# Kernel tuning notes

Measured on AMD Instinct MI355X. Metric: run time of the kernel, lower is better.

## Reference

```python
import jax, jax.numpy as jnp
import numpy as np

NO = 16          # config['Max_Object']
NT = 8           # config['Max_Time']
FEAT = 512       # config['feat_dims']
VIS_IN = 2048
TGT = 24


def setup_inputs() -> dict:
    key = jax.random.key(0)
    ks = jax.random.split(key, 10)
    b = 16
    N = NT * 2 * NO  # 256
    s = lambda k, *sh: jax.random.normal(k, sh, dtype=jnp.float32) * 0.02
    return {
        "src": jax.random.normal(ks[0], (b, 1, 1, N, VIS_IN), dtype=jnp.float32),
        "tgt_rel": jax.random.randint(ks[1], (b * NT * NO * NO,), 0, TGT, dtype=jnp.int64),
        "w1": s(ks[2], VIS_IN, FEAT), "b1": jnp.zeros((FEAT,), jnp.float32),
        "w2": s(ks[3], FEAT, FEAT),   "b2": jnp.zeros((FEAT,), jnp.float32),
        "wf": s(ks[4], FEAT, FEAT),   "bf": jnp.zeros((FEAT,), jnp.float32),
        "wr": s(ks[5], 2 * FEAT, TGT), "br": jnp.zeros((TGT,), jnp.float32),
    }


def reference(src, tgt_rel, w1, b1, w2, b2, wf, bf, wr, br):
    b = src.shape[0]
    BT = b * NT
    # src[:, 0, 0, :, :] -> (b, N, D) -> (b*NT, 2*NO, D); take visual part [:2048]
    x = src[:, 0, 0, :, :].reshape(BT, 2 * NO, -1)[:, :, :VIS_IN]
    # fc_vis: MLP 2048 -> FEAT -> FEAT
    h = jnp.maximum(x @ w1 + b1, 0.0) @ w2 + b2          # (BT, 2NO, FEAT)
    node_feats = h @ wf + bf                             # fc_fusion
    # vectorized replacement of the NOxNO python double loop:
    # edge[:, i*NO + (j-NO), :] = cat(node[:, i], node[:, j])  for i<NO<=j
    subj = jnp.broadcast_to(node_feats[:, :NO, None, :], (BT, NO, NO, FEAT))
    obj = jnp.broadcast_to(node_feats[:, None, NO:, :], (BT, NO, NO, FEAT))
    edge_feats = jnp.concatenate([subj, obj], axis=-1).reshape(BT, NO * NO, 2 * FEAT)
    out = (edge_feats @ wr + br).reshape(-1, TGT)        # fc_rel
    tgt = tgt_rel.reshape(-1)
    w_cls = jnp.asarray([1.0] + [100.0] * (TGT - 1), dtype=out.dtype)
    logp = jax.nn.log_softmax(out, axis=-1)
    nll = -jnp.take_along_axis(logp, tgt[:, None], axis=1)[:, 0]
    ww = w_cls[tgt]
    loss = jnp.sum(ww * nll) / jnp.sum(ww)  # torch weighted cross_entropy (mean)
    return out, tgt, loss
```

## Files before the change

### kernel.cpp

```cpp
#include <hip/hip_runtime.h>
#include <cstddef>
#include <cstdint>

#define NOBJ   16
#define FEAT   512
#define VIS    2048
#define NTGT   24
#define MROWS  4096
#define EROWS  32768

typedef __attribute__((ext_vector_type(8))) short short8;
typedef __attribute__((ext_vector_type(4))) float f32x4;
typedef __attribute__((ext_vector_type(16))) float f32x16;

__device__ __forceinline__ unsigned short f2bf(float f) {
    union { float f; unsigned int i; } v; v.f = f;
    const unsigned int x = v.i;
    return (unsigned short)((x + 0x7fffu + ((x >> 16) & 1u)) >> 16);
}

__device__ __forceinline__ void gload16(const unsigned short* g, unsigned short* l) {
    __builtin_amdgcn_global_load_lds(
        (const __attribute__((address_space(1))) unsigned int*)(const void*)g,
        (__attribute__((address_space(3))) unsigned int*)(void*)l, 16, 0, 0);
}

__global__ __launch_bounds__(256)
void prep1(const float* __restrict__ w1, unsigned short* __restrict__ w1t,
           const float* __restrict__ wf, const float* __restrict__ bfv,
           const float* __restrict__ wr, float* __restrict__ t1,
           const float* __restrict__ src, unsigned short* __restrict__ srcb,
           float* __restrict__ P) {
    __shared__ float shbuf[FEAT * NTGT];
    const int b   = blockIdx.x;
    const int tid = threadIdx.x;
    if (b < 1024) {
        float (*tile)[33] = (float(*)[33])shbuf;
        const int k0 = (b & 63) * 32;
        const int n0 = (b >> 6) * 32;
        const int tx = tid & 31, ty = tid >> 5;
        #pragma unroll
        for (int r = 0; r < 32; r += 8)
            tile[ty + r][tx] = w1[(size_t)(k0 + ty + r) * FEAT + n0 + tx];
        __syncthreads();
        #pragma unroll
        for (int r = 0; r < 32; r += 8)
            w1t[(size_t)(n0 + ty + r) * VIS + k0 + tx] = f2bf(tile[tx][ty + r]);
    } else if (b < 1154) {
        const int bb = b - 1024;
        const int h  = bb & 1;
        const float* wrh = wr + (size_t)h * FEAT * NTGT;
        for (int idx = tid; idx < FEAT * NTGT; idx += 256)
            shbuf[idx] = wrh[idx];
        __syncthreads();
        const int c    = tid & 31;
        const int krow = (bb >> 1) * 8 + (tid >> 5);
        if (krow > 512) return;
        const float* rowp = (krow < 512) ? (wf + (size_t)krow * FEAT) : bfv;
        const int ce = (c < NTGT) ? c : NTGT - 1;
        float s = 0.f;
        #pragma unroll 8
        for (int j = 0; j < FEAT; ++j)
            s = fmaf(rowp[j], shbuf[j * NTGT + ce], s);
        if (c < NTGT) t1[((size_t)h * 513 + krow) * 32 + c] = s;
    } else if (b < 2178) {
        const int bb = b - 1154;
        #pragma unroll
        for (int q = 0; q < 4; ++q) {
            const size_t i = (size_t)bb * 8192 + q * 2048 + tid * 8;
            const float4 a = *reinterpret_cast<const float4*>(src + i);
            const float4 c = *reinterpret_cast<const float4*>(src + i + 4);
            short8 o;
            o[0] = (short)f2bf(a.x); o[1] = (short)f2bf(a.y);
            o[2] = (short)f2bf(a.z); o[3] = (short)f2bf(a.w);
            o[4] = (short)f2bf(c.x); o[5] = (short)f2bf(c.y);
            o[6] = (short)f2bf(c.z); o[7] = (short)f2bf(c.w);
            *reinterpret_cast<short8*>(srcb + i) = o;
        }
    } else {
        const int bb = b - 2178;
        P[(size_t)bb * 256 + tid] = 0.f;
    }
}

__global__ __launch_bounds__(256)
void prep2(const float* __restrict__ w2, const float* __restrict__ b2,
           const float* __restrict__ t1, unsigned short* __restrict__ wABt,
           float* __restrict__ biasAB) {
    __shared__ float shbuf[FEAT * NTGT];
    const int b   = blockIdx.x;
    const int tid = threadIdx.x;
    const int h   = b & 1;
    for (int idx = tid; idx < FEAT * NTGT; idx += 256) {
        const int row = idx / NTGT, col = idx - row * NTGT;
        shbuf[idx] = t1[((size_t)h * 513 + row) * 32 + col];
    }
    __syncthreads();
    const int c = tid & 31;
    const int r = (b >> 1) * 8 + (tid >> 5);
    if (r > 512) return;
    const float* rowp = (r < 512) ? (w2 + (size_t)r * FEAT) : b2;
    const int ce = (c < NTGT) ? c : NTGT - 1;
    float s = 0.f;
    #pragma unroll 8
    for (int k = 0; k < FEAT; ++k)
        s = fmaf(rowp[k], shbuf[k * NTGT + ce], s);
    if (c < NTGT) {
        const int q = h * NTGT + c;
        if (r < 512) wABt[(size_t)q * FEAT + r] = f2bf(s);
        else         biasAB[q] = s + t1[((size_t)h * 513 + 512) * 32 + c];
    }
}

__global__ __launch_bounds__(256)
void gemm1f(const unsigned short* __restrict__ srcb, const unsigned short* __restrict__ w1t,
            const float* __restrict__ b1, const unsigned short* __restrict__ wABt,
            float* __restrict__ P) {
    __shared__ __align__(16) unsigned short As[2][128 * 64];
    __shared__ __align__(16) unsigned short Bs[2][32 * 64];

    const int bid = blockIdx.x;
    const int xcd = bid & 7;
    const int k8  = bid >> 3;
    const int xb  = k8 & 15;
    const int yb  = (xcd << 2) | (k8 >> 4);
    const int m0 = yb * 128;
    const int n0 = xb * 32;

    const int tid  = threadIdx.x;
    const int lane = tid & 63;
    const int wid  = tid >> 6;

    const int aRow = tid >> 3, aCd = (tid & 7) ^ (aRow & 7);
    const int bN   = tid >> 3, bCd = (tid & 7) ^ (bN & 7);
    const size_t aOff = (size_t)(m0 + aRow) * VIS + (aCd << 3);
    const size_t bOff = (size_t)(n0 + bN) * VIS + (bCd << 3);
    const int ldsWb = (wid * 64) << 3;

    f32x16 acc = {};

    #pragma unroll
    for (int q = 0; q < 4; ++q)
        gload16(srcb + aOff + (size_t)q * 32 * VIS, &As[0][(q * 256) * 8 + ldsWb]);
    gload16(w1t + bOff, &Bs[0][ldsWb]);
    __syncthreads();

    int cur = 0;
    for (int t = 0; t < VIS / 64; ++t) {
        if (t + 1 < VIS / 64) {
            const int kn = (t + 1) * 64;
            #pragma unroll
            for (int q = 0; q < 4; ++q)
                gload16(srcb + aOff + (size_t)q * 32 * VIS + kn,
                        &As[cur ^ 1][(q * 256) * 8 + ldsWb]);
            gload16(w1t + bOff + kn, &Bs[cur ^ 1][ldsWb]);
        }
        #pragma unroll
        for (int k2 = 0; k2 < 4; ++k2) {
            const int chunk = (k2 << 1) + (lane >> 5);
            short8 af, bf8;
            {
                const int row = wid * 32 + (lane & 31);
                const int cw  = chunk ^ (row & 7);
                af = *reinterpret_cast<const short8*>(&As[cur][(row << 6) + (cw << 3)]);
            }
            {
                const int n  = lane & 31;
                const int cw = chunk ^ (n & 7);
                bf8 = *reinterpret_cast<const short8*>(&Bs[cur][(n << 6) + (cw << 3)]);
            }
            acc = __builtin_amdgcn_mfma_f32_32x32x16_bf16(af, bf8, acc, 0, 0, 0);
        }
        __syncthreads();
        cur ^= 1;
    }

    unsigned short* Ht = &As[0][0];
    {
        const float bias = b1[n0 + (lane & 31)];
        #pragma unroll
        for (int r = 0; r < 16; ++r) {
            const int row = wid * 32 + (r & 3) + ((r >> 2) << 3) + ((lane >> 5) << 2);
            const float v = fmaxf(acc[r] + bias, 0.f);
            Ht[row * 40 + (lane & 31)] = f2bf(v);
        }
    }
    __syncthreads();

    short8 bq[3];
    #pragma unroll
    for (int t3 = 0; t3 < 3; ++t3)
        bq[t3] = *reinterpret_cast<const short8*>(
            wABt + (size_t)(t3 * 16 + (lane & 15)) * FEAT + n0 + ((lane >> 4) << 3));

    const f32x4 pz = {0.f, 0.f, 0.f, 0.f};
    #pragma unroll
    for (int fr = 0; fr < 2; ++fr) {
        short8 aep;
        {
            const int m = wid * 32 + fr * 16 + (lane & 15);
            aep = *reinterpret_cast<const short8*>(&Ht[m * 40 + ((lane >> 4) << 3)]);
        }
        #pragma unroll
        for (int t3 = 0; t3 < 3; ++t3) {
            f32x4 pp = __builtin_amdgcn_mfma_f32_16x16x32_bf16(aep, bq[t3], pz, 0, 0, 0);
            const int q  = t3 * 16 + (lane & 15);
            const int mb = m0 + wid * 32 + fr * 16 + ((lane >> 4) << 2);
            #pragma unroll
            for (int r = 0; r < 4; ++r)
                atomicAdd(&P[(size_t)(mb + r) * 64 + q], pp[r]);
        }
    }
}

__global__ __launch_bounds__(256)
void out_loss_kernel(const float* __restrict__ P, const float* __restrict__ br,
                     const float* __restrict__ biasAB, const int* __restrict__ tgt,
                     float* __restrict__ out, float* __restrict__ out_tgt,
                     float* __restrict__ partials) {
    __shared__ float sm[32][49];
    const int bt  = blockIdx.x;
    const int tid = threadIdx.x;
    for (int idx = tid; idx < 32 * 48; idx += 256) {
        const int row = idx / 48, col = idx - row * 48;
        sm[row][col] = P[(size_t)(bt * 32 + row) * 64 + col];
    }
    __syncthreads();

    const int r  = bt * 256 + tid;
    const int i  = tid >> 4, j = tid & 15;
    const int tg = tgt[r];

    float vals[NTGT];
    float mx = -1e30f, vtg = 0.f;
    #pragma unroll
    for (int t = 0; t < NTGT; ++t) {
        const float cv = br[t] + biasAB[t] + biasAB[24 + t];
        const float v  = sm[i][t] + sm[16 + j][24 + t] + cv;
        vals[t] = v;
        mx = fmaxf(mx, v);
        if (t == tg) vtg = v;
    }
    float se = 0.f;
    #pragma unroll
    for (int t = 0; t < NTGT; ++t) se += expf(vals[t] - mx);
    const float lse = mx + logf(se);

    float4* o4 = reinterpret_cast<float4*>(out + (size_t)r * NTGT);
    #pragma unroll
    for (int q = 0; q < 6; ++q)
        o4[q] = make_float4(vals[q * 4], vals[q * 4 + 1], vals[q * 4 + 2], vals[q * 4 + 3]);
    out_tgt[r] = (float)tg;

    const float wcl = (tg == 0) ? 1.f : 100.f;
    float p1 = wcl * (lse - vtg);
    float p2 = wcl;
    #pragma unroll
    for (int off = 32; off > 0; off >>= 1) {
        p1 += __shfl_down(p1, off);
        p2 += __shfl_down(p2, off);
    }
    __shared__ float s1[4], s2[4];
    const int lane = tid & 63, wv = tid >> 6;
    if (lane == 0) { s1[wv] = p1; s2[wv] = p2; }
    __syncthreads();
    if (tid == 0) {
        partials[bt]       = s1[0] + s1[1] + s1[2] + s1[3];
        partials[128 + bt] = s2[0] + s2[1] + s2[2] + s2[3];
    }
}

__global__ void final_loss(const float* __restrict__ partials, float* __restrict__ loss) {
    const int t = threadIdx.x;
    float a = partials[t] + partials[t + 64];
    float b = partials[128 + t] + partials[192 + t];
    #pragma unroll
    for (int off = 32; off > 0; off >>= 1) {
        a += __shfl_down(a, off);
        b += __shfl_down(b, off);
    }
    if (t == 0) loss[0] = a / b;
}

extern "C" void kernel_launch(void* const* d_in, const int* in_sizes, int n_in,
                              void* d_out, int out_size, void* d_ws, size_t ws_size,
                              hipStream_t stream) {
    const float* src = (const float*)d_in[0];
    const int*   tgt = (const int*)d_in[1];
    const float* w1  = (const float*)d_in[2];
    const float* b1  = (const float*)d_in[3];
    const float* w2  = (const float*)d_in[4];
    const float* b2  = (const float*)d_in[5];
    const float* wf  = (const float*)d_in[6];
    const float* bfv = (const float*)d_in[7];
    const float* wr  = (const float*)d_in[8];
    const float* br  = (const float*)d_in[9];

    float* ws = (float*)d_ws;
    unsigned short* w1t   = (unsigned short*)(ws);
    unsigned short* srcb  = (unsigned short*)(ws + 524288);
    float*          t1    = ws + 4718592;
    unsigned short* wABt  = (unsigned short*)(ws + 4751424);
    float*          biasAB = ws + 4763712;
    float*          P     = ws + 4763776;
    float*          parts = ws + 5025920;

    float* out_logits = (float*)d_out;
    float* out_tgt    = out_logits + (size_t)EROWS * NTGT;
    float* out_lossp  = out_tgt + EROWS;

    prep1<<<3202, 256, 0, stream>>>(w1, w1t, wf, bfv, wr, t1, src, srcb, P);
    prep2<<<130, 256, 0, stream>>>(w2, b2, t1, wABt, biasAB);
    gemm1f<<<512, 256, 0, stream>>>(srcb, w1t, b1, wABt, P);
    out_loss_kernel<<<128, 256, 0, stream>>>(P, br, biasAB, tgt,
                                             out_logits, out_tgt, parts);
    final_loss<<<1, 64, 0, stream>>>(parts, out_lossp);
}
```

Measured before the change: 163.6 us.

## Triple-buffer gemm1f K loop and vectorize weight-fold matvecs in prep kernels

The main GEMM's K loop moves from double to triple buffering with global_load_lds. It now waits on vmcnt and a raw s_barrier, so two stages of loads stay in flight while MFMAs run on the current buffer. Separately, the wf·wr and w2·t1 precompute matvecs are reworked so each thread computes 4 output columns using float4 row loads and f32x4 LDS reads. That lets the prep kernels use many fewer blocks (26 instead of 130), cutting redundant LDS fills of the 48KB weight slab. The cost is more LDS per GEMM block, which may lower occupancy, plus fragile manual waitcnt accounting.

Measured after the change: 160.2 us. 2.1% less time.

```diff
diff --git a/kernel.cpp b/kernel.cpp
--- a/kernel.cpp
+++ b/kernel.cpp
@@ -46,25 +46,34 @@
         #pragma unroll
         for (int r = 0; r < 32; r += 8)
             w1t[(size_t)(n0 + ty + r) * VIS + k0 + tx] = f2bf(tile[tx][ty + r]);
-    } else if (b < 1154) {
+    } else if (b < 1050) {
         const int bb = b - 1024;
-        const int h  = bb & 1;
+        const int h  = bb / 13, blk = bb % 13;
         const float* wrh = wr + (size_t)h * FEAT * NTGT;
         for (int idx = tid; idx < FEAT * NTGT; idx += 256)
             shbuf[idx] = wrh[idx];
         __syncthreads();
-        const int c    = tid & 31;
-        const int krow = (bb >> 1) * 8 + (tid >> 5);
-        if (krow > 512) return;
-        const float* rowp = (krow < 512) ? (wf + (size_t)krow * FEAT) : bfv;
-        const int ce = (c < NTGT) ? c : NTGT - 1;
-        float s = 0.f;
-        #pragma unroll 8
-        for (int j = 0; j < FEAT; ++j)
-            s = fmaf(rowp[j], shbuf[j * NTGT + ce], s);
-        if (c < NTGT) t1[((size_t)h * 513 + krow) * 32 + c] = s;
-    } else if (b < 2178) {
-        const int bb = b - 1154;
+        if (tid < 252) {
+            const int krow = blk * 42 + tid / 6;
+            const int cg   = tid % 6;
+            if (krow <= 512) {
+                const float* rowp = (krow < 512) ? (wf + (size_t)krow * FEAT) : bfv;
+                const f32x4* shb4 = (const f32x4*)shbuf;
+                f32x4 p = {0.f, 0.f, 0.f, 0.f};
+                #pragma unroll 4
+                for (int j = 0; j < FEAT; j += 4) {
+                    const float4 a = *reinterpret_cast<const float4*>(rowp + j);
+                    const f32x4 w0 = shb4[(j + 0) * 6 + cg];
+                    const f32x4 w1v = shb4[(j + 1) * 6 + cg];
+                    const f32x4 w2v = shb4[(j + 2) * 6 + cg];
+                    const f32x4 w3v = shb4[(j + 3) * 6 + cg];
+                    p += a.x * w0 + a.y * w1v + a.z * w2v + a.w * w3v;
+                }
+                *reinterpret_cast<f32x4*>(t1 + ((size_t)h * 513 + krow) * 32 + cg * 4) = p;
+            }
+        }
+    } else if (b < 2074) {
+        const int bb = b - 1050;
         #pragma unroll
         for (int q = 0; q < 4; ++q) {
             const size_t i = (size_t)bb * 8192 + q * 2048 + tid * 8;
@@ -78,7 +87,7 @@
             *reinterpret_cast<short8*>(srcb + i) = o;
         }
     } else {
-        const int bb = b - 2178;
+        const int bb = b - 2074;
         P[(size_t)bb * 256 + tid] = 0.f;
     }
 }
@@ -90,25 +99,33 @@
     __shared__ float shbuf[FEAT * NTGT];
     const int b   = blockIdx.x;
     const int tid = threadIdx.x;
-    const int h   = b & 1;
+    const int h   = b / 13, blk = b % 13;
     for (int idx = tid; idx < FEAT * NTGT; idx += 256) {
         const int row = idx / NTGT, col = idx - row * NTGT;
         shbuf[idx] = t1[((size_t)h * 513 + row) * 32 + col];
     }
     __syncthreads();
-    const int c = tid & 31;
-    const int r = (b >> 1) * 8 + (tid >> 5);
+    if (tid >= 252) return;
+    const int r  = blk * 42 + tid / 6;
+    const int cg = tid % 6;
     if (r > 512) return;
     const float* rowp = (r < 512) ? (w2 + (size_t)r * FEAT) : b2;
-    const int ce = (c < NTGT) ? c : NTGT - 1;
-    float s = 0.f;
-    #pragma unroll 8
-    for (int k = 0; k < FEAT; ++k)
-        s = fmaf(rowp[k], shbuf[k * NTGT + ce], s);
-    if (c < NTGT) {
-        const int q = h * NTGT + c;
-        if (r < 512) wABt[(size_t)q * FEAT + r] = f2bf(s);
-        else         biasAB[q] = s + t1[((size_t)h * 513 + 512) * 32 + c];
+    const f32x4* shb4 = (const f32x4*)shbuf;
+    f32x4 p = {0.f, 0.f, 0.f, 0.f};
+    #pragma unroll 4
+    for (int k = 0; k < FEAT; k += 4) {
+        const float4 a = *reinterpret_cast<const float4*>(rowp + k);
+        const f32x4 w0 = shb4[(k + 0) * 6 + cg];
+        const f32x4 w1v = shb4[(k + 1) * 6 + cg];
+        const f32x4 w2v = shb4[(k + 2) * 6 + cg];
+        const f32x4 w3v = shb4[(k + 3) * 6 + cg];
+        p += a.x * w0 + a.y * w1v + a.z * w2v + a.w * w3v;
+    }
+    #pragma unroll
+    for (int e = 0; e < 4; ++e) {
+        const int q = h * NTGT + cg * 4 + e;
+        if (r < 512) wABt[(size_t)q * FEAT + r] = f2bf(p[e]);
+        else         biasAB[q] = p[e] + t1[((size_t)h * 513 + 512) * 32 + cg * 4 + e];
     }
 }
 
@@ -116,8 +133,8 @@
 void gemm1f(const unsigned short* __restrict__ srcb, const unsigned short* __restrict__ w1t,
             const float* __restrict__ b1, const unsigned short* __restrict__ wABt,
             float* __restrict__ P) {
-    __shared__ __align__(16) unsigned short As[2][128 * 64];
-    __shared__ __align__(16) unsigned short Bs[2][32 * 64];
+    __shared__ __align__(16) unsigned short As[3][128 * 64];
+    __shared__ __align__(16) unsigned short Bs[3][32 * 64];
 
     const int bid = blockIdx.x;
     const int xcd = bid & 7;
@@ -139,22 +156,27 @@
 
     f32x16 acc = {};
 
-    #pragma unroll
-    for (int q = 0; q < 4; ++q)
-        gload16(srcb + aOff + (size_t)q * 32 * VIS, &As[0][(q * 256) * 8 + ldsWb]);
-    gload16(w1t + bOff, &Bs[0][ldsWb]);
-    __syncthreads();
-
-    int cur = 0;
-    for (int t = 0; t < VIS / 64; ++t) {
-        if (t + 1 < VIS / 64) {
-            const int kn = (t + 1) * 64;
-            #pragma unroll
-            for (int q = 0; q < 4; ++q)
-                gload16(srcb + aOff + (size_t)q * 32 * VIS + kn,
-                        &As[cur ^ 1][(q * 256) * 8 + ldsWb]);
-            gload16(w1t + bOff + kn, &Bs[cur ^ 1][ldsWb]);
-        }
+    #define STAGE(tt, bi)                                                        \
+        do {                                                                     \
+            const int kn_ = (tt) * 64;                                           \
+            _Pragma("unroll")                                                    \
+            for (int q_ = 0; q_ < 4; ++q_)                                       \
+                gload16(srcb + aOff + (size_t)q_ * 32 * VIS + kn_,               \
+                        &As[bi][(q_ * 256) * 8 + ldsWb]);                        \
+            gload16(w1t + bOff + kn_, &Bs[bi][ldsWb]);                           \
+        } while (0)
+
+    STAGE(0, 0);
+    STAGE(1, 1);
+
+    const int NT = VIS / 64;
+    for (int t = 0; t < NT; ++t) {
+        if (t < NT - 1) asm volatile("s_waitcnt vmcnt(5)" ::: "memory");
+        else            asm volatile("s_waitcnt vmcnt(0)" ::: "memory");
+        __builtin_amdgcn_s_barrier();
+        asm volatile("" ::: "memory");
+        if (t + 2 < NT) STAGE(t + 2, (t + 2) % 3);
+        const int cb = t % 3;
         #pragma unroll
         for (int k2 = 0; k2 < 4; ++k2) {
             const int chunk = (k2 << 1) + (lane >> 5);
@@ -162,18 +184,17 @@
             {
                 const int row = wid * 32 + (lane & 31);
                 const int cw  = chunk ^ (row & 7);
-                af = *reinterpret_cast<const short8*>(&As[cur][(row << 6) + (cw << 3)]);
+                af = *reinterpret_cast<const short8*>(&As[cb][(row << 6) + (cw << 3)]);
             }
             {
                 const int n  = lane & 31;
                 const int cw = chunk ^ (n & 7);
-                bf8 = *reinterpret_cast<const short8*>(&Bs[cur][(n << 6) + (cw << 3)]);
+                bf8 = *reinterpret_cast<const short8*>(&Bs[cb][(n << 6) + (cw << 3)]);
             }
             acc = __builtin_amdgcn_mfma_f32_32x32x16_bf16(af, bf8, acc, 0, 0, 0);
         }
-        __syncthreads();
-        cur ^= 1;
-    }
+    }
+    #undef STAGE
 
     unsigned short* Ht = &As[0][0];
     {
@@ -309,8 +330,8 @@
     float* out_tgt    = out_logits + (size_t)EROWS * NTGT;
     float* out_lossp  = out_tgt + EROWS;
 
-    prep1<<<3202, 256, 0, stream>>>(w1, w1t, wf, bfv, wr, t1, src, srcb, P);
-    prep2<<<130, 256, 0, stream>>>(w2, b2, t1, wABt, biasAB);
+    prep1<<<3098, 256, 0, stream>>>(w1, w1t, wf, bfv, wr, t1, src, srcb, P);
+    prep2<<<26, 256, 0, stream>>>(w2, b2, t1, wABt, biasAB);
     gemm1f<<<512, 256, 0, stream>>>(srcb, w1t, b1, wABt, P);
     out_loss_kernel<<<128, 256, 0, stream>>>(P, br, biasAB, tgt,
                                              out_logits, out_tgt, parts);
```
